# Kernel optimization log

Measured on AMD Instinct MI355X. Metric: run time of the kernel, lower is better.

The kernel has to match this reference:

```python
import jax, jax.numpy as jnp
import numpy as np

EPS = 1e-6
LAMBDA_INIT = 0.8
ROPE_BASE = 10000.0
NUM_HEADS = 8


def rmsnorm(x, w):
    rms = jnp.sqrt(jnp.mean(x * x, axis=-1, keepdims=True) + EPS)
    return x / rms * w


def apply_rope(x):
    # Faithful to source: positions are taken along dim -2 of x.
    # Here x has shape (B, r, H, d), so rotation angle is indexed by HEAD index
    # (this mirrors the original torch code, where apply_rope is called on
    # (B, seq, H, d) tensors and uses x.shape[-2] == H for positions).
    d = x.shape[-1]
    half = d // 2  # d is even (head_dim=64)
    pos = jnp.arange(x.shape[-2])
    dim_idx = jnp.arange(half, dtype=x.dtype)
    freqs = 1.0 / (ROPE_BASE ** (dim_idx / half))
    angles = pos[:, None].astype(jnp.float32) * freqs  # (H, half)
    cos, sin = jnp.cos(angles), jnp.sin(angles)
    x1, x2 = x[..., :half], x[..., half:2 * half]
    return jnp.concatenate([x1 * cos - x2 * sin, x1 * sin + x2 * cos], axis=-1)


def linterp(x, out_size):
    # torch F.interpolate(mode='linear', align_corners=False) along axis 1 of (B, L, C)
    in_size = x.shape[1]
    scale = in_size / out_size
    coords = jnp.clip((jnp.arange(out_size) + 0.5) * scale - 0.5, 0.0, in_size - 1)
    lo = jnp.floor(coords).astype(jnp.int32)
    hi = jnp.minimum(lo + 1, in_size - 1)
    w = (coords - lo)[None, :, None].astype(x.dtype)
    return x[:, lo] * (1 - w) + x[:, hi] * w


def setup_inputs() -> dict:
    key = jax.random.key(0)
    ks = jax.random.split(key, 12)
    B, L, C = 4, 4096, 1024
    H = NUM_HEADS
    d = C // (2 * H)  # 64
    s = 0.02
    return {
        "x": jax.random.normal(ks[0], (B, L, C), jnp.float32),
        "Wq": jax.random.normal(ks[1], (C, C), jnp.float32) * s,
        "Wk": jax.random.normal(ks[2], (C, C), jnp.float32) * s,
        "Wv": jax.random.normal(ks[3], (C, C), jnp.float32) * s,
        "Wo": jax.random.normal(ks[4], (C, C), jnp.float32) * s,
        "q_norm_w": 1.0 + jax.random.normal(ks[5], (d,), jnp.float32) * s,
        "k_norm_w": 1.0 + jax.random.normal(ks[6], (d,), jnp.float32) * s,
        "head_norm_w": 1.0 + jax.random.normal(ks[7], (2 * d,), jnp.float32) * s,
        "lambda_q1": jax.random.normal(ks[8], (d,), jnp.float32) * 0.1,
        "lambda_k1": jax.random.normal(ks[9], (d,), jnp.float32) * 0.1,
        "lambda_q2": jax.random.normal(ks[10], (d,), jnp.float32) * 0.1,
        "lambda_k2": jax.random.normal(ks[11], (d,), jnp.float32) * 0.1,
    }


def reference(x, Wq, Wk, Wv, Wo, q_norm_w, k_norm_w, head_norm_w,
              lambda_q1, lambda_k1, lambda_q2, lambda_k2):
    B, L, C = x.shape
    H = NUM_HEADS
    d = C // (2 * H)
    scale = d ** -0.5
    r = max(1, int(L ** 0.75))  # 512 for L=4096

    xd = linterp(x, r)  # (B, r, C)

    q = (xd @ Wq.T).reshape(B, r, H, 2, d)
    k = (xd @ Wk.T).reshape(B, r, H, 2, d)
    v = (xd @ Wv.T).reshape(B, r, H, 2 * d)

    q1 = apply_rope(rmsnorm(q[..., 0, :], q_norm_w))
    q2 = apply_rope(rmsnorm(q[..., 1, :], q_norm_w))
    k1 = apply_rope(rmsnorm(k[..., 0, :], k_norm_w))
    k2 = apply_rope(rmsnorm(k[..., 1, :], k_norm_w))

    # (B, H, r, d)
    q1, q2 = jnp.swapaxes(q1, 1, 2), jnp.swapaxes(q2, 1, 2)
    k1, k2 = jnp.swapaxes(k1, 1, 2), jnp.swapaxes(k2, 1, 2)
    v = jnp.swapaxes(v, 1, 2)  # (B, H, r, 2d)

    lam = (jnp.exp(jnp.sum(lambda_q1 * lambda_k1))
           - jnp.exp(jnp.sum(lambda_q2 * lambda_k2)) + LAMBDA_INIT)

    attn1 = jax.nn.softmax(jnp.einsum('bhqd,bhkd->bhqk', q1, k1) * scale, axis=-1)
    attn2 = jax.nn.softmax(jnp.einsum('bhqd,bhkd->bhqk', q2, k2) * scale, axis=-1)
    diff = jnp.einsum('bhqk,bhkd->bhqd', attn1 - lam * attn2, v)  # (B,H,r,2d)

    diff = jnp.swapaxes(diff, 1, 2)  # (B, r, H, 2d)
    diff = rmsnorm(diff, head_norm_w) * (1.0 - LAMBDA_INIT)
    lowrank_out = jax.nn.silu(diff.reshape(B, r, C) @ Wo.T)
    full_out = linterp(lowrank_out, L)
    return (full_out, lowrank_out)
```

## Files before the change

kernel.cpp:

```cpp
#include <hip/hip_runtime.h>

typedef __bf16 bf16_t;
typedef __bf16 bf16x8 __attribute__((ext_vector_type(8)));
typedef __bf16 bf16x4 __attribute__((ext_vector_type(4)));
typedef float  f32x4  __attribute__((ext_vector_type(4)));

#define MFMA16(a,b,c) __builtin_amdgcn_mfma_f32_16x16x32_bf16((a),(b),(c),0,0,0)

#define NB 4
#define LL 4096
#define CC 1024
#define HH 8
#define RR 512

__global__ void k_prep(const float* __restrict__ x,
                       const float* __restrict__ w0, const float* __restrict__ w1,
                       const float* __restrict__ w2, const float* __restrict__ w3,
                       bf16_t* __restrict__ wbf, bf16_t* __restrict__ xd) {
  int bid = blockIdx.x;
  if (bid < 4096) {
    int y = bid >> 10;
    const float* src = (y == 0) ? w0 : (y == 1) ? w1 : (y == 2) ? w2 : w3;
    int idx = (bid & 1023) * 256 + threadIdx.x;
    f32x4 v = *(const f32x4*)&src[(size_t)idx * 4];
    bf16x4 o;
#pragma unroll
    for (int j = 0; j < 4; ++j) o[j] = (bf16_t)v[j];
    *(bf16x4*)&wbf[(size_t)y * 1048576 + (size_t)idx * 4] = o;
  } else {
    int idx = (bid - 4096) * 256 + threadIdx.x;
    int c4  = idx & 255;
    int row = idx >> 8;
    int b = row >> 9, i = row & 511;
    const float* p0 = x + (size_t)(b * LL + 8 * i + 3) * CC + c4 * 4;
    f32x4 a = *(const f32x4*)p0;
    f32x4 bb = *(const f32x4*)(p0 + CC);
    bf16x4 o;
#pragma unroll
    for (int j = 0; j < 4; ++j) o[j] = (bf16_t)(0.5f * (a[j] + bb[j]));
    *(bf16x4*)&xd[(size_t)row * CC + c4 * 4] = o;
  }
}

template <int CH>
__device__ __forceinline__ void stage_async(const bf16_t* __restrict__ g, bf16_t* __restrict__ s, int t) {
#pragma unroll
  for (int j = 0; j < CH; ++j) {
    int c = t + j * 256;
    const bf16_t* ga = g + (c >> 2) * 1024 + (c & 3) * 8;
    bf16_t* la = s + c * 8;
    __builtin_amdgcn_global_load_lds((const __attribute__((address_space(1))) void*)ga,
                                     (__attribute__((address_space(3))) void*)la, 16, 0, 0);
  }
}

template <int MODE, int BM, int BN>
__global__ __launch_bounds__(256) void k_gemm(const bf16_t* __restrict__ A,
                                              const bf16_t* __restrict__ wbf,
                                              const float* __restrict__ qw,
                                              const float* __restrict__ kw,
                                              bf16_t* __restrict__ q1, bf16_t* __restrict__ q2,
                                              bf16_t* __restrict__ k1, bf16_t* __restrict__ k2,
                                              bf16_t* __restrict__ vt, float* __restrict__ outF) {
  __shared__ bf16_t sA[3][BM * 32];
  __shared__ bf16_t sB[3][BN * 32];
  const int z = (MODE == 0) ? blockIdx.z : 3;
  const bf16_t* W = wbf + (size_t)z * (1u << 20);
  int t = threadIdx.x;
  int lane = t & 63, w = t >> 6;
  int wr = w >> 1, wc = w & 1;
  int lr = lane & 15, quad = lane >> 4;
  int m0 = blockIdx.y * BM, n0 = blockIdx.x * BN;
  constexpr int NI = BM / 32, NJ = BN / 32;
  f32x4 acc[NI][NJ] = {};
  const bf16_t* Ab = A + (size_t)m0 * 1024;
  const bf16_t* Wb = W + (size_t)n0 * 1024;

  stage_async<BM / 64>(Ab, sA[0], t);
  stage_async<BN / 64>(Wb, sB[0], t);
  stage_async<BM / 64>(Ab + 32, sA[1], t);
  stage_async<BN / 64>(Wb + 32, sB[1], t);

  int cur = 0, stg = 2;
#pragma unroll 1
  for (int it = 0; it < 32; ++it) {
    if (it < 31) {
      constexpr int L = BM / 64 + BN / 64;
      if constexpr (L == 2) asm volatile("s_waitcnt vmcnt(2) lgkmcnt(0)" ::: "memory");
      else if constexpr (L == 3) asm volatile("s_waitcnt vmcnt(3) lgkmcnt(0)" ::: "memory");
      else asm volatile("s_waitcnt vmcnt(4) lgkmcnt(0)" ::: "memory");
    } else {
      asm volatile("s_waitcnt vmcnt(0) lgkmcnt(0)" ::: "memory");
    }
    __builtin_amdgcn_s_barrier();
    if (it < 30) {
      stage_async<BM / 64>(Ab + (it + 2) * 32, sA[stg], t);
      stage_async<BN / 64>(Wb + (it + 2) * 32, sB[stg], t);
    }
    const bf16_t* cA = sA[cur];
    const bf16_t* cB = sB[cur];
    bf16x8 af[NI], bfr[NJ];
#pragma unroll
    for (int i = 0; i < NI; ++i) af[i] = *(const bf16x8*)&cA[(wr * (BM / 2) + i * 16 + lr) * 32 + quad * 8];
#pragma unroll
    for (int j = 0; j < NJ; ++j) bfr[j] = *(const bf16x8*)&cB[(wc * (BN / 2) + j * 16 + lr) * 32 + quad * 8];
#pragma unroll
    for (int i = 0; i < NI; ++i)
#pragma unroll
      for (int j = 0; j < NJ; ++j)
        acc[i][j] = MFMA16(af[i], bfr[j], acc[i][j]);
    cur = (cur == 2) ? 0 : cur + 1;
    stg = (stg == 2) ? 0 : stg + 1;
  }

  if constexpr (MODE == 1) {
#pragma unroll
    for (int i = 0; i < NI; ++i)
#pragma unroll
      for (int j = 0; j < NJ; ++j) {
        int row0 = m0 + wr * (BM / 2) + i * 16 + quad * 4;
        int col  = n0 + wc * (BN / 2) + j * 16 + lr;
#pragma unroll
        for (int rg = 0; rg < 4; ++rg) {
          float v = acc[i][j][rg];
          outF[(size_t)(row0 + rg) * 1024 + col] = v / (1.f + __expf(-v));
        }
      }
    return;
  } else {
    if (z == 2) {
#pragma unroll
      for (int i = 0; i < NI; ++i)
#pragma unroll
        for (int j = 0; j < NJ; ++j) {
          int row0 = m0 + wr * (BM / 2) + i * 16 + quad * 4;
          int col  = n0 + wc * (BN / 2) + j * 16 + lr;
          int b = row0 >> 9, ii = row0 & 511;
          int h = col >> 7, nn = col & 127;
          bf16x4 pk;
#pragma unroll
          for (int rg = 0; rg < 4; ++rg) pk[rg] = (bf16_t)acc[i][j][rg];
          *(bf16x4*)&vt[(size_t)((b * HH + h) * 128 + nn) * 512 + ii] = pk;
        }
      return;
    }
    const float* nw = z ? kw : qw;
    int colbase = n0 + wc * (BN / 2);
    int h = colbase >> 7;
    int slot = (colbase >> 6) & 1;
    bf16_t* dst = (z == 0) ? (slot ? q2 : q1) : (slot ? k2 : k1);
    float qs = (z == 0) ? 0.125f : 1.0f;
    float w0 = nw[lr], w1 = nw[16 + lr], w2 = nw[32 + lr], w3 = nw[48 + lr];
    const float nlog = -13.287712379549449f / 32.f;
    float f0 = exp2f((float)lr * nlog);
    float f1 = exp2f((float)(16 + lr) * nlog);
    float sn0, cs0, sn1, cs1;
    __sincosf((float)h * f0, &sn0, &cs0);
    __sincosf((float)h * f1, &sn1, &cs1);
#pragma unroll
    for (int i = 0; i < NI; ++i) {
#pragma unroll
      for (int rg = 0; rg < 4; ++rg) {
        float v0 = acc[i][0][rg], v1 = acc[i][1][rg], v2 = acc[i][2][rg], v3 = acc[i][3][rg];
        float ss = v0 * v0 + v1 * v1 + v2 * v2 + v3 * v3;
#pragma unroll
        for (int m = 1; m <= 8; m <<= 1) ss += __shfl_xor(ss, m);
        float rinv = qs / sqrtf(ss * (1.f / 64.f) + 1e-6f);
        float n0v = v0 * rinv * w0, n1v = v1 * rinv * w1, n2v = v2 * rinv * w2, n3v = v3 * rinv * w3;
        float o0 = n0v * cs0 - n2v * sn0;
        float o1 = n1v * cs1 - n3v * sn1;
        float o2 = n0v * sn0 + n2v * cs0;
        float o3 = n1v * sn1 + n3v * cs1;
        int row = m0 + wr * (BM / 2) + i * 16 + quad * 4 + rg;
        int b = row >> 9, seq = row & 511;
        size_t base = ((size_t)((b * HH + h) * RR + seq)) * 64;
        dst[base + lr]      = (bf16_t)o0;
        dst[base + 16 + lr] = (bf16_t)o1;
        dst[base + 32 + lr] = (bf16_t)o2;
        dst[base + 48 + lr] = (bf16_t)o3;
      }
    }
  }
}

__global__ __launch_bounds__(256) void k_attn(const bf16_t* __restrict__ q1, const bf16_t* __restrict__ q2,
                                              const bf16_t* __restrict__ k1, const bf16_t* __restrict__ k2,
                                              const bf16_t* __restrict__ vt,
                                              const float* __restrict__ lq1, const float* __restrict__ lk1,
                                              const float* __restrict__ lq2, const float* __restrict__ lk2,
                                              const float* __restrict__ hw, bf16_t* __restrict__ anorm) {
  __shared__ bf16_t P[16 * 520];
  __shared__ float Sm1[4][16], Sl1[4][16], Sm2[4][16], Sl2[4][16], Sq[4][16];
  int t = threadIdx.x;
  int lane = t & 63, w = t >> 6;
  int lr = lane & 15, quad = lane >> 4;
  int qt = blockIdx.x, bh = blockIdx.y;
  int b = bh >> 3, h = bh & 7;

  float t1 = lq1[lane] * lk1[lane];
  float t2 = lq2[lane] * lk2[lane];
#pragma unroll
  for (int m = 1; m <= 32; m <<= 1) { t1 += __shfl_xor(t1, m); t2 += __shfl_xor(t2, m); }
  float lam = expf(t1) - expf(t2) + 0.8f;

  const bf16_t* q1b = q1 + (size_t)(bh * RR + qt * 16) * 64;
  const bf16_t* q2b = q2 + (size_t)(bh * RR + qt * 16) * 64;
  const bf16_t* k1b = k1 + (size_t)bh * RR * 64;
  const bf16_t* k2b = k2 + (size_t)bh * RR * 64;
  const bf16_t* vtb = vt + (size_t)bh * 128 * 512;

  bf16x8 a1[2], a2[2];
#pragma unroll
  for (int kk = 0; kk < 2; ++kk) {
    a1[kk] = *(const bf16x8*)&q1b[lr * 64 + kk * 32 + quad * 8];
    a2[kk] = *(const bf16x8*)&q2b[lr * 64 + kk * 32 + quad * 8];
  }

  f32x4 s1[8], s2[8];
#pragma unroll
  for (int kt = 0; kt < 8; ++kt) {
    const bf16_t* kr = k1b + (size_t)((w * 8 + kt) * 16 + lr) * 64 + quad * 8;
    f32x4 a = {};
    a = MFMA16(a1[0], *(const bf16x8*)kr, a);
    a = MFMA16(a1[1], *(const bf16x8*)(kr + 32), a);
    s1[kt] = a;
  }
#pragma unroll
  for (int kt = 0; kt < 8; ++kt) {
    const bf16_t* kr = k2b + (size_t)((w * 8 + kt) * 16 + lr) * 64 + quad * 8;
    f32x4 a = {};
    a = MFMA16(a2[0], *(const bf16x8*)kr, a);
    a = MFMA16(a2[1], *(const bf16x8*)(kr + 32), a);
    s2[kt] = a;
  }
  float m1[4] = {-3e38f, -3e38f, -3e38f, -3e38f}, m2[4] = {-3e38f, -3e38f, -3e38f, -3e38f};
#pragma unroll
  for (int kt = 0; kt < 8; ++kt)
#pragma unroll
    for (int rg = 0; rg < 4; ++rg) { m1[rg] = fmaxf(m1[rg], s1[kt][rg]); m2[rg] = fmaxf(m2[rg], s2[kt][rg]); }
#pragma unroll
  for (int m = 1; m <= 8; m <<= 1)
#pragma unroll
    for (int rg = 0; rg < 4; ++rg) { m1[rg] = fmaxf(m1[rg], __shfl_xor(m1[rg], m)); m2[rg] = fmaxf(m2[rg], __shfl_xor(m2[rg], m)); }
  float l1[4] = {}, l2[4] = {};
#pragma unroll
  for (int kt = 0; kt < 8; ++kt)
#pragma unroll
    for (int rg = 0; rg < 4; ++rg) {
      float e1 = __expf(s1[kt][rg] - m1[rg]); s1[kt][rg] = e1; l1[rg] += e1;
      float e2 = __expf(s2[kt][rg] - m2[rg]); s2[kt][rg] = e2; l2[rg] += e2;
    }
#pragma unroll
  for (int m = 1; m <= 8; m <<= 1)
#pragma unroll
    for (int rg = 0; rg < 4; ++rg) { l1[rg] += __shfl_xor(l1[rg], m); l2[rg] += __shfl_xor(l2[rg], m); }
  if (lr == 0) {
#pragma unroll
    for (int rg = 0; rg < 4; ++rg) {
      int r = quad * 4 + rg;
      Sm1[w][r] = m1[rg]; Sl1[w][r] = l1[rg];
      Sm2[w][r] = m2[rg]; Sl2[w][r] = l2[rg];
    }
  }
  __syncthreads();
  float sc1[4], sc2[4];
#pragma unroll
  for (int rg = 0; rg < 4; ++rg) {
    int r = quad * 4 + rg;
    float gm1 = fmaxf(fmaxf(Sm1[0][r], Sm1[1][r]), fmaxf(Sm1[2][r], Sm1[3][r]));
    float L1 = Sl1[0][r] * __expf(Sm1[0][r] - gm1) + Sl1[1][r] * __expf(Sm1[1][r] - gm1)
             + Sl1[2][r] * __expf(Sm1[2][r] - gm1) + Sl1[3][r] * __expf(Sm1[3][r] - gm1);
    sc1[rg] = __expf(m1[rg] - gm1) / L1;
    float gm2 = fmaxf(fmaxf(Sm2[0][r], Sm2[1][r]), fmaxf(Sm2[2][r], Sm2[3][r]));
    float L2 = Sl2[0][r] * __expf(Sm2[0][r] - gm2) + Sl2[1][r] * __expf(Sm2[1][r] - gm2)
             + Sl2[2][r] * __expf(Sm2[2][r] - gm2) + Sl2[3][r] * __expf(Sm2[3][r] - gm2);
    sc2[rg] = lam * __expf(m2[rg] - gm2) / L2;
  }
#pragma unroll
  for (int kt = 0; kt < 8; ++kt)
#pragma unroll
    for (int rg = 0; rg < 4; ++rg) {
      float v = s1[kt][rg] * sc1[rg] - s2[kt][rg] * sc2[rg];
      P[(quad * 4 + rg) * 520 + (w * 8 + kt) * 16 + lr] = (bf16_t)v;
    }
  __syncthreads();
  f32x4 accO[2] = {};
#pragma unroll
  for (int ks = 0; ks < 16; ++ks) {
    bf16x8 pf = *(bf16x8*)&P[lr * 520 + ks * 32 + quad * 8];
#pragma unroll
    for (int j = 0; j < 2; ++j) {
      int nt = w * 2 + j;
      bf16x8 vf = *(const bf16x8*)&vtb[(size_t)(nt * 16 + lr) * 512 + ks * 32 + quad * 8];
      accO[j] = MFMA16(pf, vf, accO[j]);
    }
  }
  float ssr[4] = {};
#pragma unroll
  for (int j = 0; j < 2; ++j)
#pragma unroll
    for (int rg = 0; rg < 4; ++rg) ssr[rg] += accO[j][rg] * accO[j][rg];
#pragma unroll
  for (int m = 1; m <= 8; m <<= 1)
#pragma unroll
    for (int rg = 0; rg < 4; ++rg) ssr[rg] += __shfl_xor(ssr[rg], m);
  if (lr == 0) {
#pragma unroll
    for (int rg = 0; rg < 4; ++rg) Sq[w][quad * 4 + rg] = ssr[rg];
  }
  __syncthreads();
#pragma unroll
  for (int j = 0; j < 2; ++j) {
    int nt = w * 2 + j;
    float wcol = hw[nt * 16 + lr];
#pragma unroll
    for (int rg = 0; rg < 4; ++rg) {
      int r = quad * 4 + rg;
      float tot = Sq[0][r] + Sq[1][r] + Sq[2][r] + Sq[3][r];
      float rinv = 0.2f / sqrtf(tot * (1.f / 128.f) + 1e-6f);
      int i = qt * 16 + r;
      anorm[(size_t)(b * RR + i) * 1024 + h * 128 + nt * 16 + lr] = (bf16_t)(accO[j][rg] * rinv * wcol);
    }
  }
}

__global__ void k_up(const float* __restrict__ lrk, float* __restrict__ out) {
  int j = blockIdx.x;
  int b = blockIdx.y;
  int c = threadIdx.x * 4;
  float coord = 0.125f * (float)j - 0.4375f;
  coord = fminf(fmaxf(coord, 0.f), 511.f);
  int lo = (int)floorf(coord);
  int hi = lo + 1 < 511 ? lo + 1 : 511;
  float w = coord - (float)lo;
  f32x4 a = *(const f32x4*)&lrk[(size_t)(b * RR + lo) * CC + c];
  f32x4 bb = *(const f32x4*)&lrk[(size_t)(b * RR + hi) * CC + c];
  f32x4 o;
#pragma unroll
  for (int t = 0; t < 4; ++t) o[t] = a[t] * (1.f - w) + bb[t] * w;
  *(f32x4*)&out[(size_t)(b * LL + j) * CC + c] = o;
}

extern "C" void kernel_launch(void* const* d_in, const int* in_sizes, int n_in,
                              void* d_out, int out_size, void* d_ws, size_t ws_size,
                              hipStream_t stream) {
  (void)in_sizes; (void)n_in; (void)out_size; (void)ws_size;
  const float* x   = (const float*)d_in[0];
  const float* Wq  = (const float*)d_in[1];
  const float* Wk  = (const float*)d_in[2];
  const float* Wv  = (const float*)d_in[3];
  const float* Wo  = (const float*)d_in[4];
  const float* qw  = (const float*)d_in[5];
  const float* kw  = (const float*)d_in[6];
  const float* hw  = (const float*)d_in[7];
  const float* lq1 = (const float*)d_in[8];
  const float* lk1 = (const float*)d_in[9];
  const float* lq2 = (const float*)d_in[10];
  const float* lk2 = (const float*)d_in[11];
  float* out = (float*)d_out;

  char* ws = (char*)d_ws;
  bf16_t* wbf   = (bf16_t*)(ws);
  bf16_t* xd    = (bf16_t*)(ws + (8u << 20));
  bf16_t* vt    = (bf16_t*)(ws + (12u << 20));
  bf16_t* q1    = (bf16_t*)(ws + (16u << 20));
  bf16_t* q2    = (bf16_t*)(ws + (18u << 20));
  bf16_t* k1    = (bf16_t*)(ws + (20u << 20));
  bf16_t* k2    = (bf16_t*)(ws + (22u << 20));
  bf16_t* anorm = (bf16_t*)(ws + (24u << 20));

  float* lowrank = out + (size_t)NB * LL * CC;

  k_prep<<<6144, 256, 0, stream>>>(x, Wq, Wk, Wv, Wo, wbf, xd);
  k_gemm<0, 64, 128><<<dim3(8, 32, 3), 256, 0, stream>>>(xd, wbf, qw, kw, q1, q2, k1, k2, vt, nullptr);
  k_attn<<<dim3(32, 32), 256, 0, stream>>>(q1, q2, k1, k2, vt, lq1, lk1, lq2, lk2, hw, anorm);
  k_gemm<1, 64, 64><<<dim3(16, 32, 1), 256, 0, stream>>>(anorm, wbf, qw, kw, nullptr, nullptr, nullptr, nullptr, nullptr, lowrank);
  k_up<<<dim3(4096, 4), 256, 0, stream>>>(lowrank, out);
}
```

Before: 232.9 us.

## Remap block indices for XCD locality and stage V transpose through LDS

Flattens all grids to 1D and remaps block IDs so consecutive tasks land on the same XCD (bid&7 interleave), aiming to improve L2 reuse of shared A/W tiles, K/V rows and lowrank rows on the multi-die MI355X. The V-projection epilogue now transposes the tile through shared memory and writes 16-byte coalesced rows into vt, replacing scattered 8-byte stores. Adds two block barriers in the V path and depends on the assumption that hardware dispatches blocks round-robin across 8 XCDs.

```diff
diff --git a/kernel.cpp b/kernel.cpp
--- a/kernel.cpp
+++ b/kernel.cpp
@@ -62,24 +62,36 @@
                                               bf16_t* __restrict__ q1, bf16_t* __restrict__ q2,
                                               bf16_t* __restrict__ k1, bf16_t* __restrict__ k2,
                                               bf16_t* __restrict__ vt, float* __restrict__ outF) {
-  __shared__ bf16_t sA[3][BM * 32];
-  __shared__ bf16_t sB[3][BN * 32];
-  const int z = (MODE == 0) ? blockIdx.z : 3;
+  __shared__ __align__(16) char smem[3 * (BM * 64) + 3 * (BN * 64)];
+  bf16_t* sA = (bf16_t*)smem;
+  bf16_t* sB = (bf16_t*)(smem + 3 * (BM * 64));
+
+  int bid = blockIdx.x;
+  int z, m0, n0;
+  if constexpr (MODE == 0) {
+    int task = (bid & 7) * 96 + (bid >> 3);
+    z = task >> 8;
+    int rem = task & 255;
+    m0 = (rem >> 3) * BM; n0 = (rem & 7) * BN;
+  } else {
+    int task = (bid & 7) * 64 + (bid >> 3);
+    z = 3;
+    m0 = (task >> 4) * BM; n0 = (task & 15) * BN;
+  }
   const bf16_t* W = wbf + (size_t)z * (1u << 20);
   int t = threadIdx.x;
   int lane = t & 63, w = t >> 6;
   int wr = w >> 1, wc = w & 1;
   int lr = lane & 15, quad = lane >> 4;
-  int m0 = blockIdx.y * BM, n0 = blockIdx.x * BN;
   constexpr int NI = BM / 32, NJ = BN / 32;
   f32x4 acc[NI][NJ] = {};
   const bf16_t* Ab = A + (size_t)m0 * 1024;
   const bf16_t* Wb = W + (size_t)n0 * 1024;
 
-  stage_async<BM / 64>(Ab, sA[0], t);
-  stage_async<BN / 64>(Wb, sB[0], t);
-  stage_async<BM / 64>(Ab + 32, sA[1], t);
-  stage_async<BN / 64>(Wb + 32, sB[1], t);
+  stage_async<BM / 64>(Ab, sA, t);
+  stage_async<BN / 64>(Wb, sB, t);
+  stage_async<BM / 64>(Ab + 32, sA + BM * 32, t);
+  stage_async<BN / 64>(Wb + 32, sB + BN * 32, t);
 
   int cur = 0, stg = 2;
 #pragma unroll 1
@@ -94,11 +106,11 @@
     }
     __builtin_amdgcn_s_barrier();
     if (it < 30) {
-      stage_async<BM / 64>(Ab + (it + 2) * 32, sA[stg], t);
-      stage_async<BN / 64>(Wb + (it + 2) * 32, sB[stg], t);
-    }
-    const bf16_t* cA = sA[cur];
-    const bf16_t* cB = sB[cur];
+      stage_async<BM / 64>(Ab + (it + 2) * 32, sA + stg * (BM * 32), t);
+      stage_async<BN / 64>(Wb + (it + 2) * 32, sB + stg * (BN * 32), t);
+    }
+    const bf16_t* cA = sA + cur * (BM * 32);
+    const bf16_t* cB = sB + cur * (BN * 32);
     bf16x8 af[NI], bfr[NJ];
 #pragma unroll
     for (int i = 0; i < NI; ++i) af[i] = *(const bf16x8*)&cA[(wr * (BM / 2) + i * 16 + lr) * 32 + quad * 8];
@@ -129,19 +141,30 @@
     return;
   } else {
     if (z == 2) {
+      __syncthreads();
+      bf16_t* tp = (bf16_t*)smem;
 #pragma unroll
       for (int i = 0; i < NI; ++i)
 #pragma unroll
         for (int j = 0; j < NJ; ++j) {
-          int row0 = m0 + wr * (BM / 2) + i * 16 + quad * 4;
-          int col  = n0 + wc * (BN / 2) + j * 16 + lr;
-          int b = row0 >> 9, ii = row0 & 511;
-          int h = col >> 7, nn = col & 127;
+          int iiw = wr * (BM / 2) + i * 16 + quad * 4;
+          int nn  = wc * (BN / 2) + j * 16 + lr;
           bf16x4 pk;
 #pragma unroll
           for (int rg = 0; rg < 4; ++rg) pk[rg] = (bf16_t)acc[i][j][rg];
-          *(bf16x4*)&vt[(size_t)((b * HH + h) * 128 + nn) * 512 + ii] = pk;
+          *(bf16x4*)&tp[nn * 68 + iiw] = pk;
         }
+      __syncthreads();
+      int b = m0 >> 9, ii0 = m0 & 511;
+      int h = n0 >> 7;
+      size_t basev = (size_t)((b * HH + h) * 128) * 512 + ii0;
+#pragma unroll
+      for (int r = 0; r < 4; ++r) {
+        int nn = r * 32 + (t >> 3);
+        int k8 = (t & 7) * 8;
+        bf16x8 v = *(bf16x8*)&tp[nn * 68 + k8];
+        *(bf16x8*)&vt[basev + (size_t)nn * 512 + k8] = v;
+      }
       return;
     }
     const float* nw = z ? kw : qw;
@@ -194,7 +217,8 @@
   int t = threadIdx.x;
   int lane = t & 63, w = t >> 6;
   int lr = lane & 15, quad = lane >> 4;
-  int qt = blockIdx.x, bh = blockIdx.y;
+  int task = (blockIdx.x & 7) * 128 + (blockIdx.x >> 3);
+  int qt = task & 31, bh = task >> 5;
   int b = bh >> 3, h = bh & 7;
 
   float t1 = lq1[lane] * lk1[lane];
@@ -325,8 +349,9 @@
 }
 
 __global__ void k_up(const float* __restrict__ lrk, float* __restrict__ out) {
-  int j = blockIdx.x;
-  int b = blockIdx.y;
+  int task = (blockIdx.x & 7) * 2048 + (blockIdx.x >> 3);
+  int j = task & 4095;
+  int b = task >> 12;
   int c = threadIdx.x * 4;
   float coord = 0.125f * (float)j - 0.4375f;
   coord = fminf(fmaxf(coord, 0.f), 511.f);
@@ -372,8 +397,8 @@
   float* lowrank = out + (size_t)NB * LL * CC;
 
   k_prep<<<6144, 256, 0, stream>>>(x, Wq, Wk, Wv, Wo, wbf, xd);
-  k_gemm<0, 64, 128><<<dim3(8, 32, 3), 256, 0, stream>>>(xd, wbf, qw, kw, q1, q2, k1, k2, vt, nullptr);
-  k_attn<<<dim3(32, 32), 256, 0, stream>>>(q1, q2, k1, k2, vt, lq1, lk1, lq2, lk2, hw, anorm);
-  k_gemm<1, 64, 64><<<dim3(16, 32, 1), 256, 0, stream>>>(anorm, wbf, qw, kw, nullptr, nullptr, nullptr, nullptr, nullptr, lowrank);
-  k_up<<<dim3(4096, 4), 256, 0, stream>>>(lowrank, out);
-}
+  k_gemm<0, 64, 128><<<768, 256, 0, stream>>>(xd, wbf, qw, kw, q1, q2, k1, k2, vt, nullptr);
+  k_attn<<<1024, 256, 0, stream>>>(q1, q2, k1, k2, vt, lq1, lk1, lq2, lk2, hw, anorm);
+  k_gemm<1, 64, 64><<<512, 256, 0, stream>>>(anorm, wbf, qw, kw, nullptr, nullptr, nullptr, nullptr, nullptr, lowrank);
+  k_up<<<16384, 256, 0, stream>>>(lowrank, out);
+}
```

After: 221.3 us. 1.05x faster.
